# Kernel optimization log

Hardware: AMD Instinct MI355X
Metric: run time of the kernel (lower is better)

Reference implementation:

```python
import jax, jax.numpy as jnp
import numpy as np

B, S, D = 4, 1024, 2048
H, KVH = 32, 8
HD = D // H            # 64
KVD = HD * KVH         # 512
RANK, ALPHA = 16, 32
LORA_SCALE = ALPHA / RANK


def setup_inputs() -> dict:
    key = jax.random.key(0)
    ks = jax.random.split(key, 14)
    x = jax.random.normal(ks[0], (B, S, D), dtype=jnp.float32)
    # RoPE tables (llama-style complex freqs as cos/sin)
    inv = 1.0 / (10000.0 ** (np.arange(0, HD, 2, dtype=np.float32) / HD))
    t = np.arange(S, dtype=np.float32)
    ang = np.outer(t, inv)  # [S, HD//2]
    freqs_cos = jnp.asarray(np.cos(ang))
    freqs_sin = jnp.asarray(np.sin(ang))
    s = 0.02
    Wq = jax.random.normal(ks[1], (D, D), dtype=jnp.float32) * s
    Wk = jax.random.normal(ks[2], (D, KVD), dtype=jnp.float32) * s
    Wv = jax.random.normal(ks[3], (D, KVD), dtype=jnp.float32) * s
    Wo = jax.random.normal(ks[4], (D, D), dtype=jnp.float32) * s
    qA = jax.random.normal(ks[5], (D, RANK), dtype=jnp.float32) * s
    qB = jax.random.normal(ks[6], (RANK, D), dtype=jnp.float32) * s
    kA = jax.random.normal(ks[7], (D, RANK), dtype=jnp.float32) * s
    kB = jax.random.normal(ks[8], (RANK, KVD), dtype=jnp.float32) * s
    vA = jax.random.normal(ks[9], (D, RANK), dtype=jnp.float32) * s
    vB = jax.random.normal(ks[10], (RANK, KVD), dtype=jnp.float32) * s
    return {"x": x, "freqs_cos": freqs_cos, "freqs_sin": freqs_sin,
            "Wq": Wq, "Wk": Wk, "Wv": Wv, "Wo": Wo,
            "qA": qA, "qB": qB, "kA": kA, "kB": kB, "vA": vA, "vB": vB}


def _rope(t, cos, sin):
    # t: [b, s, h, hd]; cos/sin: [s, hd//2]
    b, s, h, hd = t.shape
    t2 = t.reshape(b, s, h, hd // 2, 2)
    x0, x1 = t2[..., 0], t2[..., 1]
    c = cos[None, :, None, :]
    sn = sin[None, :, None, :]
    r0 = x0 * c - x1 * sn
    r1 = x0 * sn + x1 * c
    return jnp.stack([r0, r1], axis=-1).reshape(b, s, h, hd)


def reference(x, freqs_cos, freqs_sin, Wq, Wk, Wv, Wo, qA, qB, kA, kB, vA, vB):
    b, s, _ = x.shape
    # QKV projections + LoRA deltas
    q = x @ Wq + (x @ qA) @ qB * LORA_SCALE   # [b,s,D]
    k = x @ Wk + (x @ kA) @ kB * LORA_SCALE   # [b,s,KVD]
    v = x @ Wv + (x @ vA) @ vB * LORA_SCALE   # [b,s,KVD]
    q = q.reshape(b, s, H, HD)
    k = k.reshape(b, s, KVH, HD)
    v = v.reshape(b, s, KVH, HD)
    q = _rope(q, freqs_cos, freqs_sin)
    k = _rope(k, freqs_cos, freqs_sin)
    # GQA attention without materializing repeated K/V:
    rep = H // KVH
    qg = q.reshape(b, s, KVH, rep, HD)
    scale = 1.0 / jnp.sqrt(jnp.asarray(HD, dtype=x.dtype))
    scores = jnp.einsum('bsgrd,btgd->bgrst', qg, k) * scale  # [b,kvh,rep,s,s]
    causal = jnp.tril(jnp.ones((s, s), dtype=bool))
    scores = jnp.where(causal[None, None, None], scores, jnp.finfo(scores.dtype).min)
    attn = jax.nn.softmax(scores, axis=-1)
    ctx = jnp.einsum('bgrst,btgd->bsgrd', attn, v).reshape(b, s, D)
    return ctx @ Wo
```

## Files before the change

kernel.cpp:

```cpp
#include <hip/hip_runtime.h>

typedef unsigned short u16;
typedef unsigned int u32;
typedef __attribute__((ext_vector_type(8))) short short8;
typedef __attribute__((ext_vector_type(4))) float f32x4;
typedef __attribute__((ext_vector_type(4))) u16 u16x4;

#define LOG2E 1.4426950408889634f
#define SCL2 (0.125f * LOG2E)

static __device__ __forceinline__ float bf2f(u16 u) {
    return __uint_as_float(((unsigned)u) << 16);
}
static __device__ __forceinline__ u16 f2bf(float f) {
    unsigned u = __float_as_uint(f);
    unsigned r = (u + 0x7FFF + ((u >> 16) & 1)) >> 16;
    return (u16)r;
}
static __device__ __forceinline__ u32 cvtpk(float lo, float hi) {
    u32 r;
    asm("v_cvt_pk_bf16_f32 %0, %1, %2" : "=v"(r) : "v"(lo), "v"(hi));
    return r;
}
static __device__ __forceinline__ f32x4 mfma16(short8 a, short8 b, f32x4 c) {
    return __builtin_amdgcn_mfma_f32_16x16x32_bf16(a, b, c, 0, 0, 0);
}
static __device__ __forceinline__ void gload_lds16(const void* g, void* l) {
    __builtin_amdgcn_global_load_lds(
        (const __attribute__((address_space(1))) void*)g,
        (__attribute__((address_space(3))) void*)l, 16, 0, 0);
}

#define GBAR() do { asm volatile("" ::: "memory"); __builtin_amdgcn_s_barrier(); asm volatile("" ::: "memory"); } while (0)
#define LGW()  do { asm volatile("s_waitcnt lgkmcnt(0)" ::: "memory"); __builtin_amdgcn_sched_barrier(0); } while (0)

__global__ void cast_pack_kernel(const float* __restrict__ x, u16* __restrict__ xb,
                                 const float* __restrict__ cosb, const float* __restrict__ sinb,
                                 u32* __restrict__ tbl) {
    if (blockIdx.x >= 2048) {
        const int i = (blockIdx.x - 2048) * 1024 + threadIdx.x * 4;
#pragma unroll
        for (int j = 0; j < 4; ++j)
            tbl[i + j] = (u32)f2bf(cosb[i + j]) | ((u32)f2bf(sinb[i + j]) << 16);
        return;
    }
    constexpr int n = 4096 * 2048;
    constexpr int stride = 2048 * 256 * 4;
    int i = (blockIdx.x * 256 + threadIdx.x) * 4;
#pragma unroll
    for (; i < n; i += stride) {
        f32x4 v = *(const f32x4*)&x[i];
        u16x4 o;
        o.x = f2bf(v.x); o.y = f2bf(v.y); o.z = f2bf(v.z); o.w = f2bf(v.w);
        *(u16x4*)&xb[i] = o;
    }
}

__global__ void prep_weights_kernel(
    const float* __restrict__ Wq, const float* __restrict__ Wk,
    const float* __restrict__ Wv, const float* __restrict__ Wo,
    const float* __restrict__ qA, const float* __restrict__ qB,
    const float* __restrict__ kA, const float* __restrict__ kB,
    const float* __restrict__ vA, const float* __restrict__ vB,
    u16* __restrict__ WqkvT, u16* __restrict__ WoT) {
    __shared__ float tile[32][33];
    __shared__ float As[32][17];
    __shared__ float Bs[16][33];
    const int id = blockIdx.x;
    const int tx = threadIdx.x, ty = threadIdx.y;
    const float *W, *A = nullptr, *Bm = nullptr;
    u16* dst;
    int C, bx, by;
    bool fold = true;
    if (id < 4096)      { W = Wq; A = qA; Bm = qB; dst = WqkvT; C = 2048; bx = id & 63; by = id >> 6; }
    else if (id < 5120) { int t = id - 4096; W = Wk; A = kA; Bm = kB; dst = WqkvT + (size_t)2048 * 2048; C = 512; bx = t & 15; by = t >> 4; }
    else if (id < 6144) { int t = id - 5120; W = Wv; A = vA; Bm = vB; dst = WqkvT + (size_t)2560 * 2048; C = 512; bx = t & 15; by = t >> 4; }
    else                { int t = id - 6144; W = Wo; dst = WoT; C = 2048; bx = t & 63; by = t >> 6; fold = false; }
    const int c0 = bx * 32, r0 = by * 32;
    tile[ty][tx] = W[(size_t)(r0 + ty) * C + c0 + tx];
    if (fold) {
        if (tx < 16) As[ty][tx] = A[(r0 + ty) * 16 + tx];
        if (ty < 16) Bs[ty][tx] = Bm[(size_t)ty * C + c0 + tx];
    }
    __syncthreads();
    float v = tile[tx][ty];
    if (fold) {
        float acc = 0.0f;
#pragma unroll
        for (int rr = 0; rr < 16; ++rr) acc += As[tx][rr] * Bs[rr][ty];
        v += 2.0f * acc;
    }
    dst[(size_t)(c0 + ty) * 2048 + r0 + tx] = f2bf(v);
}

__global__ __launch_bounds__(512) void gemm256_qkv_kernel(
    const u16* __restrict__ A, const u16* __restrict__ Bt, u16* __restrict__ Cq,
    u16* __restrict__ Ck, u16* __restrict__ Vt, const u32* __restrict__ ropetbl) {
    constexpr int K = 2048, NT = 32;
    __shared__ u16 Asl[2][256 * 64];
    __shared__ u16 Bsl[2][256 * 64];
    const int tid = threadIdx.x;
    const int wid = tid >> 6, lane = tid & 63;
    const int flat = blockIdx.x;
    const int m = ((flat & 7) << 1) + ((flat >> 3) & 1);
    const int n = flat >> 4;
    const int mbase = m * 256, nbase = n * 256;
    const int wrow = (wid >> 2) * 128, wcol = (wid & 3) * 64;
    const int fr = lane & 15, hi = lane >> 4;
    const int rs2 = fr & 7;
    f32x4 acc[8][4] = {};
    short8 Af[4][2], Bf[4][2];
    const u16* Ag = A + (size_t)mbase * K;
    const u16* Bg = Bt + (size_t)nbase * K;

    auto HT = [&](int t, int j) {
        if (t >= NT) return;
        const int buf = t & 1;
        u16* l = (j < 2) ? &Asl[buf][0] : &Bsl[buf][0];
        const u16* g = (j < 2) ? Ag : Bg;
        const int rbase = (j & 1) * 128;
#pragma unroll
        for (int p = 0; p < 2; ++p) {
            const int s = p * 512 + tid;
            const int row = rbase + (s >> 3);
            const int sl = (s & 7) ^ ((s >> 3) & 7);
            gload_lds16(&g[(size_t)row * K + t * 64 + sl * 8],
                        &l[rbase * 64 + (p * 512 + wid * 64) * 8]);
        }
    };
    auto DSA = [&](int mo, int buf) {
#pragma unroll
        for (int mi = 0; mi < 4; ++mi)
#pragma unroll
            for (int ks = 0; ks < 2; ++ks)
                Af[mi][ks] = *(const short8*)&Asl[buf][(wrow + (mo + mi) * 16 + fr) * 64 +
                                                       (((ks * 4 + hi) ^ rs2) * 8)];
    };
    auto DSB = [&](int no, int buf) {
#pragma unroll
        for (int ni = 0; ni < 2; ++ni)
#pragma unroll
            for (int ks = 0; ks < 2; ++ks)
                Bf[no + ni][ks] = *(const short8*)&Bsl[buf][(wcol + (no + ni) * 16 + fr) * 64 +
                                                            (((ks * 4 + hi) ^ rs2) * 8)];
    };
    auto MF = [&](int q) {
        const int mo = (q >> 1) * 4, no = (q & 1) * 2;
        __builtin_amdgcn_s_setprio(1);
#pragma unroll
        for (int mi = 0; mi < 4; ++mi)
#pragma unroll
            for (int ni = 0; ni < 2; ++ni)
#pragma unroll
                for (int ks = 0; ks < 2; ++ks)
                    acc[mo + mi][no + ni] = mfma16(Af[mi][ks], Bf[no + ni][ks], acc[mo + mi][no + ni]);
        __builtin_amdgcn_s_setprio(0);
    };

    HT(0, 0); HT(0, 1); HT(0, 2); HT(0, 3);
    HT(1, 0); HT(1, 1);
    asm volatile("s_waitcnt vmcnt(4)" ::: "memory");
    GBAR();

#pragma unroll 1
    for (int i = 0; i < NT / 2; ++i) {
        const int t = 2 * i;
        DSA(0, 0); DSB(0, 0); HT(t + 1, 2);
        GBAR(); LGW(); MF(0); GBAR();
        DSB(2, 0); HT(t + 1, 3);
        GBAR(); LGW(); MF(1); GBAR();
        DSA(4, 0);
        GBAR(); LGW(); MF(2); GBAR();
        HT(t + 2, 0); HT(t + 2, 1);
        GBAR(); LGW(); MF(3);
        if (t + 2 < NT) { asm volatile("s_waitcnt vmcnt(4)" ::: "memory"); }
        else            { asm volatile("s_waitcnt vmcnt(0)" ::: "memory"); }
        GBAR();
        DSA(0, 1); DSB(0, 1); HT(t + 2, 2);
        GBAR(); LGW(); MF(0); GBAR();
        DSB(2, 1); HT(t + 2, 3);
        GBAR(); LGW(); MF(1); GBAR();
        DSA(4, 1);
        GBAR(); LGW(); MF(2); GBAR();
        HT(t + 3, 0); HT(t + 3, 1);
        GBAR(); LGW(); MF(3);
        if (t + 3 < NT)          { asm volatile("s_waitcnt vmcnt(4)" ::: "memory"); }
        else if (i < NT / 2 - 1) { asm volatile("s_waitcnt vmcnt(0)" ::: "memory"); }
        GBAR();
    }

    const int rb = mbase + wrow + (hi << 2);
    const int cb = nbase + wcol + fr;
    if (nbase >= 2560) {
        const int cc = cb - 2560;
#pragma unroll
        for (int mi = 0; mi < 8; ++mi)
#pragma unroll
            for (int ni = 0; ni < 4; ++ni) {
                const int feat = cc + ni * 16;
                u16x4 w;
#pragma unroll
                for (int j = 0; j < 4; ++j) w[j] = f2bf(acc[mi][ni][j]);
                *(u16x4*)&Vt[(size_t)feat * 4096 + rb + mi * 16] = w;
            }
        return;
    }
    u16* C;
    int cs, cc;
    float scale;
    if (nbase < 2048) { C = Cq; cs = 2048; cc = cb;        scale = SCL2; }
    else              { C = Ck; cs = 512;  cc = cb - 2048; scale = 1.0f; }
    const bool odd = (lane & 1);
    const int ib = (fr >> 1);
#pragma unroll
    for (int mi = 0; mi < 8; ++mi)
#pragma unroll
        for (int j = 0; j < 4; ++j) {
            const int row = rb + mi * 16 + j;
            const u32* tr = ropetbl + (row & 1023) * 32;
            const size_t ro = (size_t)row * cs;
#pragma unroll
            for (int ni = 0; ni < 4; ++ni) {
                u32 cspk = tr[ib + 8 * ni];
                float cv = bf2f((u16)cspk), sv = bf2f((u16)(cspk >> 16));
                float v = acc[mi][ni][j];
                float p = __shfl_xor(v, 1);
                float r = odd ? (p * sv + v * cv) : (v * cv - p * sv);
                C[ro + cc + ni * 16] = f2bf(r * scale);
            }
        }
}

template <int CN>
__global__ __launch_bounds__(256) void gemm_kernel(
    const u16* __restrict__ A, const u16* __restrict__ Bt, float* __restrict__ C0, int Nn) {
    constexpr int K = 2048;
    constexpr int NT = K / 64;
    __shared__ u16 As[2][128 * 64];
    __shared__ u16 Bs[2][128 * 64];
    const int tid = threadIdx.x;
    const int wid = tid >> 6, lane = tid & 63;
    const int flat = blockIdx.y * gridDim.x + blockIdx.x;
    const int xcd = flat & 7, local = flat >> 3;
    const int mbase = (((xcd & 3) << 3) + (local & 7)) * 128;
    const int nbase = ((xcd >> 2) * CN + (local >> 3)) * 128;
    const int wrow = (wid >> 1) * 64, wcol = (wid & 1) * 64;
    const int fr = lane & 15, hi = lane >> 4;
    const int l8 = lane >> 3;
    const int swc = ((lane & 7) ^ l8) * 8;
    const int rs = fr & 7;
    f32x4 acc[4][4] = {};
    const u16* Ag = A + (size_t)mbase * K;
    const u16* Bg = Bt + (size_t)nbase * K;

    auto STAGE = [&](int kt, int buf) {
#pragma unroll
        for (int i = 0; i < 4; ++i) {
            const int r8 = (i * 4 + wid) * 8;
            gload_lds16(&Ag[(size_t)(r8 + l8) * K + kt * 64 + swc], &As[buf][r8 * 64]);
            gload_lds16(&Bg[(size_t)(r8 + l8) * K + kt * 64 + swc], &Bs[buf][r8 * 64]);
        }
    };

    STAGE(0, 0);
    for (int kt = 0; kt < NT; ++kt) {
        const int cur = kt & 1;
        if (kt < NT - 1) {
            STAGE(kt + 1, cur ^ 1);
            asm volatile("s_waitcnt vmcnt(8)" ::: "memory");
        } else {
            asm volatile("s_waitcnt vmcnt(0)" ::: "memory");
        }
        __builtin_amdgcn_s_barrier();
#pragma unroll
        for (int ks = 0; ks < 2; ++ks) {
            short8 af[4], bfr[4];
#pragma unroll
            for (int i = 0; i < 4; ++i) {
                const int arow = wrow + i * 16 + fr;
                const int brow = wcol + i * 16 + fr;
                af[i]  = *(const short8*)&As[cur][arow * 64 + (((ks * 4 + hi) ^ rs) * 8)];
                bfr[i] = *(const short8*)&Bs[cur][brow * 64 + (((ks * 4 + hi) ^ rs) * 8)];
            }
#pragma unroll
            for (int mi = 0; mi < 4; ++mi)
#pragma unroll
                for (int ni = 0; ni < 4; ++ni)
                    acc[mi][ni] = mfma16(af[mi], bfr[ni], acc[mi][ni]);
        }
        __builtin_amdgcn_s_barrier();
    }
    const int rb = mbase + wrow + (hi << 2);
    const int cb = nbase + wcol + fr;
#pragma unroll
    for (int mi = 0; mi < 4; ++mi)
#pragma unroll
        for (int j = 0; j < 4; ++j) {
            const size_t ro = (size_t)(rb + mi * 16 + j) * Nn;
#pragma unroll
            for (int ni = 0; ni < 4; ++ni) C0[ro + cb + ni * 16] = acc[mi][ni][j];
        }
}

template <bool DIAG>
static __device__ __forceinline__ void attn_tile_step(
    const u16* __restrict__ Ksb, const u16* __restrict__ Vsb,
    const short8* qf, f32x4* o, float& m, float& l,
    int sq, int kvb, int wid, int fr, int hi) {
    f32x4 s[4];
    const int sw = fr & 7;
#pragma unroll
    for (int mi = 0; mi < 4; ++mi) {
        if (!DIAG || mi <= wid) {
            const int row = (mi * 16 + fr) * 64;
            short8 kf0 = *(const short8*)&Ksb[row + ((hi ^ sw) * 8)];
            short8 kf1 = *(const short8*)&Ksb[row + (((4 + hi) ^ sw) * 8)];
            f32x4 z = {};
            z = mfma16(kf0, qf[0], z);
            z = mfma16(kf1, qf[1], z);
#pragma unroll
            for (int j = 0; j < 4; ++j) {
                float val = z[j];
                if (DIAG && mi == wid && (kvb + mi * 16 + hi * 4 + j > sq)) val = -3.0e38f;
                s[mi][j] = val;
            }
        } else {
            s[mi][0] = -3.0e38f; s[mi][1] = -3.0e38f;
            s[mi][2] = -3.0e38f; s[mi][3] = -3.0e38f;
        }
    }
    float pmax = fmaxf(fmaxf(fmaxf(s[0][0], s[0][1]), fmaxf(s[0][2], s[0][3])),
                       fmaxf(fmaxf(s[1][0], s[1][1]), fmaxf(s[1][2], s[1][3])));
    pmax = fmaxf(pmax, fmaxf(fmaxf(fmaxf(s[2][0], s[2][1]), fmaxf(s[2][2], s[2][3])),
                             fmaxf(fmaxf(s[3][0], s[3][1]), fmaxf(s[3][2], s[3][3]))));
    pmax = fmaxf(pmax, __shfl_xor(pmax, 16));
    pmax = fmaxf(pmax, __shfl_xor(pmax, 32));
    if (__any(pmax > m + 8.0f)) {
        const float mnew = fmaxf(m, pmax);
        const float fsc = exp2f(m - mnew);
        l *= fsc;
        m = mnew;
#pragma unroll
        for (int dn = 0; dn < 4; ++dn)
#pragma unroll
            for (int j = 0; j < 4; ++j) o[dn][j] *= fsc;
    }
    float rs = 0.0f;
    u32 pk[4][2];
#pragma unroll
    for (int mi = 0; mi < 4; ++mi) {
        float p0 = exp2f(s[mi][0] - m);
        float p1 = exp2f(s[mi][1] - m);
        float p2 = exp2f(s[mi][2] - m);
        float p3 = exp2f(s[mi][3] - m);
        rs += (p0 + p1) + (p2 + p3);
        pk[mi][0] = cvtpk(p0, p1);
        pk[mi][1] = cvtpk(p2, p3);
    }
    rs += __shfl_xor(rs, 16);
    rs += __shfl_xor(rs, 32);
    l += rs;
    const int ksmax = DIAG ? (wid >> 1) : 1;
#pragma unroll
    for (int ks = 0; ks < 2; ++ks) {
        if (ks > ksmax) continue;
        u32 w0 = pk[2 * ks][0], w2 = pk[2 * ks + 1][0];
        u32 w1 = pk[2 * ks][1], w3 = pk[2 * ks + 1][1];
        asm volatile("v_permlane32_swap_b32 %0, %1" : "+v"(w0), "+v"(w2));
        asm volatile("v_permlane16_swap_b32 %0, %1" : "+v"(w0), "+v"(w2));
        asm volatile("v_permlane32_swap_b32 %0, %1" : "+v"(w1), "+v"(w3));
        asm volatile("v_permlane16_swap_b32 %0, %1" : "+v"(w1), "+v"(w3));
        union { u32 w[4]; short8 s8; } pu;
        pu.w[0] = w0; pu.w[1] = w1; pu.w[2] = w2; pu.w[3] = w3;
        short8 pf = pu.s8;
#pragma unroll
        for (int dn = 0; dn < 4; ++dn) {
            const int row = (dn * 16 + fr) * 64;
            short8 vf = *(const short8*)&Vsb[row + (((ks * 4 + hi) ^ sw) * 8)];
            o[dn] = mfma16(vf, pf, o[dn]);
        }
    }
}

__global__ __launch_bounds__(256) void attn_kernel(
    const u16* __restrict__ q, const u16* __restrict__ k, const u16* __restrict__ vt,
    u16* __restrict__ ctx) {
    __shared__ u16 Ks[2][64 * 64];
    __shared__ u16 Vs[2][64 * 64];
    const int flat = blockIdx.x + 8 * (blockIdx.y + 16 * blockIdx.z);
    const int c = flat & 7, t = flat >> 3;
    const int jp = t & 7;
    const int grp = c + 8 * (t >> 3);
    const int hp = grp & 15, b = grp >> 4;
    const int qtA = jp, qtB = 15 - jp;
    const int h0 = hp * 2;
    const int g = hp >> 1;
    const int tid = threadIdx.x, wid = tid >> 6, lane = tid & 63;
    const int fr = lane & 15, hi = lane >> 4, fk = hi * 8;
    const int sqA = qtA * 64 + wid * 16 + fr;
    const int sqB = qtB * 64 + wid * 16 + fr;
    short8 qA0[2], qB0[2], qA1[2], qB1[2];
    {
        const u16* pa = &q[((size_t)(b * 1024 + sqA)) * 2048 + h0 * 64];
        qA0[0] = *(const short8*)&pa[fk];      qA0[1] = *(const short8*)&pa[32 + fk];
        qA1[0] = *(const short8*)&pa[64 + fk]; qA1[1] = *(const short8*)&pa[96 + fk];
        const u16* pb = &q[((size_t)(b * 1024 + sqB)) * 2048 + h0 * 64];
        qB0[0] = *(const short8*)&pb[fk];      qB0[1] = *(const short8*)&pb[32 + fk];
        qB1[0] = *(const short8*)&pb[64 + fk]; qB1[1] = *(const short8*)&pb[96 + fk];
    }
    f32x4 oA0[4] = {}, oA1[4] = {}, oB0[4] = {}, oB1[4] = {};
    float mA0 = -3.0e38f, lA0 = 0.0f, mA1 = -3.0e38f, lA1 = 0.0f;
    float mB0 = -3.0e38f, lB0 = 0.0f, mB1 = -3.0e38f, lB1 = 0.0f;
    const u16* kbase = k + ((size_t)b * 1024) * 512 + g * 64;
    const u16* vbase = vt + ((size_t)(g * 64)) * 4096 + b * 1024;
    const int l8 = lane >> 3;
    const int sw8 = ((lane & 7) ^ l8) * 8;

    auto stage = [&](int kt, int buf) {
        const u16* kg = kbase + (size_t)(kt * 64) * 512;
        const u16* vg = vbase + kt * 64;
#pragma unroll
        for (int i = 0; i < 2; ++i) {
            const int r8 = (i * 4 + wid) * 8;
            gload_lds16(&kg[(size_t)(r8 + l8) * 512 + sw8], &Ks[buf][r8 * 64]);
            gload_lds16(&vg[(size_t)(r8 + l8) * 4096 + sw8], &Vs[buf][r8 * 64]);
        }
    };

    stage(0, 0);
    for (int kt = 0; kt <= qtB; ++kt) {
        const int cur = kt & 1;
        __syncthreads();
        if (kt < qtB) stage(kt + 1, cur ^ 1);
        const int kvb = kt * 64;
        if (kt < qtA) {
            attn_tile_step<false>(Ks[cur], Vs[cur], qA0, oA0, mA0, lA0, sqA, kvb, wid, fr, hi);
            attn_tile_step<false>(Ks[cur], Vs[cur], qA1, oA1, mA1, lA1, sqA, kvb, wid, fr, hi);
        } else if (kt == qtA) {
            attn_tile_step<true>(Ks[cur], Vs[cur], qA0, oA0, mA0, lA0, sqA, kvb, wid, fr, hi);
            attn_tile_step<true>(Ks[cur], Vs[cur], qA1, oA1, mA1, lA1, sqA, kvb, wid, fr, hi);
        }
        if (kt < qtB) {
            attn_tile_step<false>(Ks[cur], Vs[cur], qB0, oB0, mB0, lB0, sqB, kvb, wid, fr, hi);
            attn_tile_step<false>(Ks[cur], Vs[cur], qB1, oB1, mB1, lB1, sqB, kvb, wid, fr, hi);
        } else {
            attn_tile_step<true>(Ks[cur], Vs[cur], qB0, oB0, mB0, lB0, sqB, kvb, wid, fr, hi);
            attn_tile_step<true>(Ks[cur], Vs[cur], qB1, oB1, mB1, lB1, sqB, kvb, wid, fr, hi);
        }
    }
    auto emit = [&](const f32x4* o, float l, int sq, int h) {
        const float linv = 1.0f / l;
        const size_t obase = ((size_t)(b * 1024 + sq)) * 2048 + h * 64;
#pragma unroll
        for (int dn = 0; dn < 4; ++dn) {
            u16x4 w;
#pragma unroll
            for (int j = 0; j < 4; ++j) w[j] = f2bf(o[dn][j] * linv);
            *(u16x4*)&ctx[obase + dn * 16 + hi * 4] = w;
        }
    };
    emit(oA0, lA0, sqA, h0);
    emit(oA1, lA1, sqA, h0 + 1);
    emit(oB0, lB0, sqB, h0);
    emit(oB1, lB1, sqB, h0 + 1);
}

extern "C" void kernel_launch(void* const* d_in, const int* in_sizes, int n_in,
                              void* d_out, int out_size, void* d_ws, size_t ws_size,
                              hipStream_t stream) {
    const float* x    = (const float*)d_in[0];
    const float* fcos = (const float*)d_in[1];
    const float* fsin = (const float*)d_in[2];
    const float* Wq   = (const float*)d_in[3];
    const float* Wk   = (const float*)d_in[4];
    const float* Wv   = (const float*)d_in[5];
    const float* Wo   = (const float*)d_in[6];
    const float* qA   = (const float*)d_in[7];
    const float* qB   = (const float*)d_in[8];
    const float* kA   = (const float*)d_in[9];
    const float* kB   = (const float*)d_in[10];
    const float* vA   = (const float*)d_in[11];
    const float* vB   = (const float*)d_in[12];
    float* out = (float*)d_out;

    char* ws = (char*)d_ws;
    size_t off = 0;
    auto alloc = [&](size_t bytes) { char* p = ws + off; off += (bytes + 255) & ~(size_t)255; return p; };
    u16* xb     = (u16*)alloc((size_t)4096 * 2048 * 2);
    u16* WqkvT  = (u16*)alloc((size_t)3072 * 2048 * 2);
    u16* WoT    = (u16*)alloc((size_t)2048 * 2048 * 2);
    u16* qbuf   = (u16*)alloc((size_t)4096 * 2048 * 2);
    u16* kbuf   = (u16*)alloc((size_t)4096 * 512 * 2);
    u16* VT2    = (u16*)alloc((size_t)512 * 4096 * 2);
    u16* ctx    = (u16*)alloc((size_t)4096 * 2048 * 2);
    u32* rtbl   = (u32*)alloc((size_t)1024 * 32 * 4);

    cast_pack_kernel<<<2080, 256, 0, stream>>>(x, xb, fcos, fsin, rtbl);
    prep_weights_kernel<<<10240, dim3(32, 32), 0, stream>>>(
        Wq, Wk, Wv, Wo, qA, qB, kA, kB, vA, vB, WqkvT, WoT);

    gemm256_qkv_kernel<<<dim3(192), 512, 0, stream>>>(xb, WqkvT, qbuf, kbuf, VT2, rtbl);

    attn_kernel<<<dim3(8, 16, 4), 256, 0, stream>>>(qbuf, kbuf, VT2, ctx);

    gemm_kernel<8><<<dim3(32, 16), 256, 0, stream>>>(ctx, WoT, out, 2048);
}
```

Measured before the change: 204.7 us.

## Retile QKV GEMM to 256x192 tiles so 256 blocks fill all CUs

Changes the fused QKV projection GEMM tile from 256x256 to 256x192, raising the grid from 192 to 256 blocks so every one of the 256 compute units gets one block. The load schedule, LDS B buffer, fragment loads and MFMA quarters are reworked for 3 column fragments per wave. The epilogue now decides per 16-column fragment whether it writes Q, K (with RoPE) or transposed V, since a 192-wide tile can straddle those boundaries. The cost is lower arithmetic intensity per tile and more global loads per MFMA.

New measurement: 194.0 us. 5.2% less time.

```diff
diff --git a/kernel.cpp b/kernel.cpp
--- a/kernel.cpp
+++ b/kernel.cpp
@@ -98,35 +98,32 @@
     u16* __restrict__ Ck, u16* __restrict__ Vt, const u32* __restrict__ ropetbl) {
     constexpr int K = 2048, NT = 32;
     __shared__ u16 Asl[2][256 * 64];
-    __shared__ u16 Bsl[2][256 * 64];
+    __shared__ u16 Bsl[2][192 * 64];
     const int tid = threadIdx.x;
     const int wid = tid >> 6, lane = tid & 63;
     const int flat = blockIdx.x;
     const int m = ((flat & 7) << 1) + ((flat >> 3) & 1);
     const int n = flat >> 4;
-    const int mbase = m * 256, nbase = n * 256;
-    const int wrow = (wid >> 2) * 128, wcol = (wid & 3) * 64;
+    const int mbase = m * 256, nbase = n * 192;
+    const int wrow = (wid >> 2) * 128, wcol = (wid & 3) * 48;
     const int fr = lane & 15, hi = lane >> 4;
     const int rs2 = fr & 7;
-    f32x4 acc[8][4] = {};
-    short8 Af[4][2], Bf[4][2];
+    f32x4 acc[8][3] = {};
+    short8 Af[4][2], Bf[3][2];
     const u16* Ag = A + (size_t)mbase * K;
     const u16* Bg = Bt + (size_t)nbase * K;
 
     auto HT = [&](int t, int j) {
         if (t >= NT) return;
         const int buf = t & 1;
-        u16* l = (j < 2) ? &Asl[buf][0] : &Bsl[buf][0];
-        const u16* g = (j < 2) ? Ag : Bg;
-        const int rbase = (j & 1) * 128;
-#pragma unroll
-        for (int p = 0; p < 2; ++p) {
-            const int s = p * 512 + tid;
-            const int row = rbase + (s >> 3);
-            const int sl = (s & 7) ^ ((s >> 3) & 7);
-            gload_lds16(&g[(size_t)row * K + t * 64 + sl * 8],
-                        &l[rbase * 64 + (p * 512 + wid * 64) * 8]);
-        }
+        const bool isA = (j < 4);
+        u16* l = isA ? &Asl[buf][0] : &Bsl[buf][0];
+        const u16* g = isA ? Ag : Bg;
+        const int rbase = (isA ? j : (j - 4)) * 64;
+        const int row = rbase + (tid >> 3);
+        const int sl = (tid & 7) ^ ((tid >> 3) & 7);
+        gload_lds16(&g[(size_t)row * K + t * 64 + sl * 8],
+                    &l[rbase * 64 + wid * 512]);
     };
     auto DSA = [&](int mo, int buf) {
 #pragma unroll
@@ -136,99 +133,95 @@
                 Af[mi][ks] = *(const short8*)&Asl[buf][(wrow + (mo + mi) * 16 + fr) * 64 +
                                                        (((ks * 4 + hi) ^ rs2) * 8)];
     };
-    auto DSB = [&](int no, int buf) {
-#pragma unroll
-        for (int ni = 0; ni < 2; ++ni)
+    auto DSB = [&](int nlo, int nhi, int buf) {
+#pragma unroll
+        for (int ni = 0; ni < 3; ++ni) {
+            if (ni < nlo || ni >= nhi) continue;
 #pragma unroll
             for (int ks = 0; ks < 2; ++ks)
-                Bf[no + ni][ks] = *(const short8*)&Bsl[buf][(wcol + (no + ni) * 16 + fr) * 64 +
-                                                            (((ks * 4 + hi) ^ rs2) * 8)];
-    };
-    auto MF = [&](int q) {
-        const int mo = (q >> 1) * 4, no = (q & 1) * 2;
+                Bf[ni][ks] = *(const short8*)&Bsl[buf][(wcol + ni * 16 + fr) * 64 +
+                                                       (((ks * 4 + hi) ^ rs2) * 8)];
+        }
+    };
+    auto MFq = [&](int mo, int nlo, int nhi) {
         __builtin_amdgcn_s_setprio(1);
 #pragma unroll
         for (int mi = 0; mi < 4; ++mi)
 #pragma unroll
-            for (int ni = 0; ni < 2; ++ni)
+            for (int ni = 0; ni < 3; ++ni) {
+                if (ni < nlo || ni >= nhi) continue;
 #pragma unroll
                 for (int ks = 0; ks < 2; ++ks)
-                    acc[mo + mi][no + ni] = mfma16(Af[mi][ks], Bf[no + ni][ks], acc[mo + mi][no + ni]);
+                    acc[mo + mi][ni] = mfma16(Af[mi][ks], Bf[ni][ks], acc[mo + mi][ni]);
+            }
         __builtin_amdgcn_s_setprio(0);
     };
 
-    HT(0, 0); HT(0, 1); HT(0, 2); HT(0, 3);
-    HT(1, 0); HT(1, 1);
+    HT(0, 0); HT(0, 1); HT(0, 2); HT(0, 3); HT(0, 4); HT(0, 5); HT(0, 6);
+    HT(1, 0); HT(1, 1); HT(1, 2); HT(1, 3);
     asm volatile("s_waitcnt vmcnt(4)" ::: "memory");
     GBAR();
 
 #pragma unroll 1
     for (int i = 0; i < NT / 2; ++i) {
         const int t = 2 * i;
-        DSA(0, 0); DSB(0, 0); HT(t + 1, 2);
-        GBAR(); LGW(); MF(0); GBAR();
-        DSB(2, 0); HT(t + 1, 3);
-        GBAR(); LGW(); MF(1); GBAR();
+        DSA(0, 0); DSB(0, 2, 0); HT(t + 1, 4); HT(t + 1, 5);
+        GBAR(); LGW(); MFq(0, 0, 2); GBAR();
+        DSB(2, 3, 0); HT(t + 1, 6);
+        GBAR(); LGW(); MFq(0, 2, 3); GBAR();
         DSA(4, 0);
-        GBAR(); LGW(); MF(2); GBAR();
-        HT(t + 2, 0); HT(t + 2, 1);
-        GBAR(); LGW(); MF(3);
+        GBAR(); LGW(); MFq(4, 0, 2); GBAR();
+        HT(t + 2, 0); HT(t + 2, 1); HT(t + 2, 2); HT(t + 2, 3);
+        GBAR(); LGW(); MFq(4, 2, 3);
         if (t + 2 < NT) { asm volatile("s_waitcnt vmcnt(4)" ::: "memory"); }
         else            { asm volatile("s_waitcnt vmcnt(0)" ::: "memory"); }
         GBAR();
-        DSA(0, 1); DSB(0, 1); HT(t + 2, 2);
-        GBAR(); LGW(); MF(0); GBAR();
-        DSB(2, 1); HT(t + 2, 3);
-        GBAR(); LGW(); MF(1); GBAR();
+        DSA(0, 1); DSB(0, 2, 1); HT(t + 2, 4); HT(t + 2, 5);
+        GBAR(); LGW(); MFq(0, 0, 2); GBAR();
+        DSB(2, 3, 1); HT(t + 2, 6);
+        GBAR(); LGW(); MFq(0, 2, 3); GBAR();
         DSA(4, 1);
-        GBAR(); LGW(); MF(2); GBAR();
-        HT(t + 3, 0); HT(t + 3, 1);
-        GBAR(); LGW(); MF(3);
+        GBAR(); LGW(); MFq(4, 0, 2); GBAR();
+        HT(t + 3, 0); HT(t + 3, 1); HT(t + 3, 2); HT(t + 3, 3);
+        GBAR(); LGW(); MFq(4, 2, 3);
         if (t + 3 < NT)          { asm volatile("s_waitcnt vmcnt(4)" ::: "memory"); }
         else if (i < NT / 2 - 1) { asm volatile("s_waitcnt vmcnt(0)" ::: "memory"); }
         GBAR();
     }
 
     const int rb = mbase + wrow + (hi << 2);
-    const int cb = nbase + wcol + fr;
-    if (nbase >= 2560) {
-        const int cc = cb - 2560;
-#pragma unroll
-        for (int mi = 0; mi < 8; ++mi)
-#pragma unroll
-            for (int ni = 0; ni < 4; ++ni) {
-                const int feat = cc + ni * 16;
+#pragma unroll
+    for (int ni = 0; ni < 3; ++ni) {
+        const int colc = nbase + wcol + ni * 16;
+        if (colc >= 2560) {
+            const int feat = colc - 2560 + fr;
+#pragma unroll
+            for (int mi = 0; mi < 8; ++mi) {
                 u16x4 w;
 #pragma unroll
                 for (int j = 0; j < 4; ++j) w[j] = f2bf(acc[mi][ni][j]);
                 *(u16x4*)&Vt[(size_t)feat * 4096 + rb + mi * 16] = w;
             }
-        return;
-    }
-    u16* C;
-    int cs, cc;
-    float scale;
-    if (nbase < 2048) { C = Cq; cs = 2048; cc = cb;        scale = SCL2; }
-    else              { C = Ck; cs = 512;  cc = cb - 2048; scale = 1.0f; }
-    const bool odd = (lane & 1);
-    const int ib = (fr >> 1);
-#pragma unroll
-    for (int mi = 0; mi < 8; ++mi)
-#pragma unroll
-        for (int j = 0; j < 4; ++j) {
-            const int row = rb + mi * 16 + j;
-            const u32* tr = ropetbl + (row & 1023) * 32;
-            const size_t ro = (size_t)row * cs;
-#pragma unroll
-            for (int ni = 0; ni < 4; ++ni) {
-                u32 cspk = tr[ib + 8 * ni];
-                float cv = bf2f((u16)cspk), sv = bf2f((u16)(cspk >> 16));
-                float v = acc[mi][ni][j];
-                float p = __shfl_xor(v, 1);
-                float r = odd ? (p * sv + v * cv) : (v * cv - p * sv);
-                C[ro + cc + ni * 16] = f2bf(r * scale);
-            }
-        }
+        } else {
+            u16* C; int cs, ccol; float scale;
+            if (colc < 2048) { C = Cq; cs = 2048; ccol = colc + fr;        scale = SCL2; }
+            else             { C = Ck; cs = 512;  ccol = colc - 2048 + fr; scale = 1.0f; }
+            const bool odd = (lane & 1);
+            const int i0 = ((colc & 63) >> 1) + (fr >> 1);
+#pragma unroll
+            for (int mi = 0; mi < 8; ++mi)
+#pragma unroll
+                for (int j = 0; j < 4; ++j) {
+                    const int row = rb + mi * 16 + j;
+                    u32 cspk = ropetbl[(row & 1023) * 32 + i0];
+                    float cv = bf2f((u16)cspk), sv = bf2f((u16)(cspk >> 16));
+                    float v = acc[mi][ni][j];
+                    float p = __shfl_xor(v, 1);
+                    float r = odd ? (p * sv + v * cv) : (v * cv - p * sv);
+                    C[(size_t)row * cs + ccol] = f2bf(r * scale);
+                }
+        }
+    }
 }
 
 template <int CN>
@@ -499,7 +492,7 @@
     prep_weights_kernel<<<10240, dim3(32, 32), 0, stream>>>(
         Wq, Wk, Wv, Wo, qA, qB, kA, kB, vA, vB, WqkvT, WoT);
 
-    gemm256_qkv_kernel<<<dim3(192), 512, 0, stream>>>(xb, WqkvT, qbuf, kbuf, VT2, rtbl);
+    gemm256_qkv_kernel<<<dim3(256), 512, 0, stream>>>(xb, WqkvT, qbuf, kbuf, VT2, rtbl);
 
     attn_kernel<<<dim3(8, 16, 4), 256, 0, stream>>>(qbuf, kbuf, VT2, ctx);
 
```
